# Optimization experiments

Hardware: AMD Instinct MI355X
Metric: run time of the kernel (lower is better)

The kernel has to match this reference:

```python
import jax, jax.numpy as jnp
import numpy as np

B, T, D = 8, 2048, 512


def setup_inputs() -> dict:
    key = jax.random.key(0)
    k1, _ = jax.random.split(key)
    h = jax.random.normal(k1, (B, T, D), dtype=jnp.float32)
    k = jnp.ones((), dtype=jnp.float32)  # scalar learned decay param, init='ones'
    return {"h": h, "k": k}


def reference(h, k):
    # h: [B, T, D], k: scalar
    Tn = h.shape[1]
    h_cum = jnp.cumsum(h, axis=1)                                   # [B,T,D]
    h_prev = jnp.pad(h[:, :-1, :], ((0, 0), (1, 0), (0, 0)))        # shift right by 1
    delta = h_cum - h_prev
    delta_mag = jnp.linalg.norm(delta, axis=-1)                      # [B,T]
    t = jnp.arange(Tn)[:, None]
    j = jnp.arange(Tn)[None, :]
    dist = jnp.abs(t - j).astype(jnp.float32)
    decay = jnp.exp(-jax.nn.softplus(k) * dist) * (j <= t)           # [T,T] causal decay
    # importance_{b,i,j} = delta_mag_{b,i} * decay_{i,j}; factor delta_mag out of einsum
    context = jnp.einsum('ij,bjd->bid', decay, h)                    # [B,T,D]
    return jnp.abs(delta_mag[..., None] * context)
```

## Files before the change

### kernel.cpp

```cpp
#include <hip/hip_runtime.h>
#include <math.h>

#define BB 8
#define TT 2048
#define DD 512
#define LL 16
#define CC (TT / LL)
#define D4 (DD / 4)

__device__ __forceinline__ float get_s(const float* kp) {
    float k = *kp;
    return (k > 20.0f) ? k : log1pf(expf(k));
}

__global__ __launch_bounds__(D4) void k1_chunk(
    const float* __restrict__ h, const float* __restrict__ kp,
    float* __restrict__ csum, float* __restrict__ cend)
{
    const int blk = blockIdx.x;
    const int b = blk / CC, c = blk % CC;
    const int tid = threadIdx.x;
    const float a = expf(-get_s(kp));

    const float4* hp = reinterpret_cast<const float4*>(h)
                     + (size_t)(b * TT + c * LL) * D4 + tid;

    float4 x[LL];
    #pragma unroll
    for (int i = 0; i < LL; i++) x[i] = hp[(size_t)i * D4];

    float sx = 0.f, sy = 0.f, sz = 0.f, sw = 0.f;
    float ex = 0.f, ey = 0.f, ez = 0.f, ew = 0.f;
    #pragma unroll
    for (int i = 0; i < LL; i++) {
        sx += x[i].x; sy += x[i].y; sz += x[i].z; sw += x[i].w;
        ex = fmaf(a, ex, x[i].x);
        ey = fmaf(a, ey, x[i].y);
        ez = fmaf(a, ez, x[i].z);
        ew = fmaf(a, ew, x[i].w);
    }
    const size_t w = (size_t)(b * CC + c) * D4 + tid;
    reinterpret_cast<float4*>(csum)[w] = make_float4(sx, sy, sz, sw);
    reinterpret_cast<float4*>(cend)[w] = make_float4(ex, ey, ez, ew);
}

__global__ __launch_bounds__(64) void k2_scan(
    const float* __restrict__ csum, const float* __restrict__ cend,
    const float* __restrict__ kp,
    float* __restrict__ coff, float* __restrict__ ccar)
{
    const int g = blockIdx.x * 64 + threadIdx.x;
    const int b = g >> 9;
    const int d = g & (DD - 1);
    const float s  = get_s(kp);
    const float aL = expf(-s * (float)LL);

    const size_t base = (size_t)b * CC * DD + d;
    float co = 0.f, cc = 0.f;
    #pragma unroll 8
    for (int c = 0; c < CC; c++) {
        const size_t idx = base + (size_t)c * DD;
        float sv = csum[idx];
        float ev = cend[idx];
        coff[idx] = co;
        ccar[idx] = cc;
        co += sv;
        cc = fmaf(aL, cc, ev);
    }
}

__global__ __launch_bounds__(D4) void k3_out(
    const float* __restrict__ h, const float* __restrict__ kp,
    const float* __restrict__ coff, const float* __restrict__ ccar,
    float* __restrict__ out)
{
    const int blk = blockIdx.x;
    const int b = blk / CC, c = blk % CC;
    const int tid = threadIdx.x;
    const int wave = tid >> 6, lane = tid & 63;
    const float a = expf(-get_s(kp));

    const int t0 = c * LL;
    const float4* hp = reinterpret_cast<const float4*>(h)
                     + (size_t)(b * TT + t0) * D4 + tid;

    float4 x[LL];
    #pragma unroll
    for (int i = 0; i < LL; i++) x[i] = hp[(size_t)i * D4];

    const size_t ci = (size_t)(b * CC + c) * D4 + tid;
    float4 co = reinterpret_cast<const float4*>(coff)[ci];
    float4 cc = reinterpret_cast<const float4*>(ccar)[ci];

    float px = 0.f, py = 0.f, pz = 0.f, pw = 0.f;
    if (t0 > 0) {
        float4 pv = hp[-(size_t)D4];
        px = pv.x; py = pv.y; pz = pv.z; pw = pv.w;
    }

    __shared__ float m2s[2][LL];
    __shared__ float mags[LL];

    float cox = co.x, coy = co.y, coz = co.z, cow = co.w;
    #pragma unroll
    for (int i = 0; i < LL; i++) {
        cox += x[i].x; coy += x[i].y; coz += x[i].z; cow += x[i].w;
        float dx = cox - px, dy = coy - py, dz = coz - pz, dw = cow - pw;
        float r = dx * dx + dy * dy + dz * dz + dw * dw;
        px = x[i].x; py = x[i].y; pz = x[i].z; pw = x[i].w;
        #pragma unroll
        for (int m = 32; m > 0; m >>= 1) r += __shfl_xor(r, m, 64);
        if (lane == 0) m2s[wave][i] = r;
    }
    __syncthreads();
    if (tid < LL) mags[tid] = sqrtf(m2s[0][tid] + m2s[1][tid]);
    __syncthreads();

    float4* op = reinterpret_cast<float4*>(out)
               + (size_t)(b * TT + t0) * D4 + tid;
    float ccx = cc.x, ccy = cc.y, ccz = cc.z, ccw = cc.w;
    #pragma unroll
    for (int i = 0; i < LL; i++) {
        ccx = fmaf(a, ccx, x[i].x);
        ccy = fmaf(a, ccy, x[i].y);
        ccz = fmaf(a, ccz, x[i].z);
        ccw = fmaf(a, ccw, x[i].w);
        float m = mags[i];
        op[(size_t)i * D4] = make_float4(fabsf(m * ccx), fabsf(m * ccy),
                                         fabsf(m * ccz), fabsf(m * ccw));
    }
}

extern "C" void kernel_launch(void* const* d_in, const int* in_sizes, int n_in,
                              void* d_out, int out_size, void* d_ws, size_t ws_size,
                              hipStream_t stream) {
    const float* h  = (const float*)d_in[0];
    const float* kp = (const float*)d_in[1];
    float* out = (float*)d_out;

    const size_t NS = (size_t)BB * CC * DD;
    float* csum = (float*)d_ws;
    float* cend = csum + NS;
    float* coff = cend + NS;
    float* ccar = coff + NS;

    k1_chunk<<<dim3(BB * CC), dim3(D4), 0, stream>>>(h, kp, csum, cend);
    k2_scan <<<dim3(BB * DD / 64), dim3(64), 0, stream>>>(csum, cend, kp, coff, ccar);
    k3_out  <<<dim3(BB * CC), dim3(D4), 0, stream>>>(h, kp, coff, ccar, out);
}
```

Baseline: 106.2 us.

## Fuse chunk, scan and output kernels into single-pass decoupled look-back scan

Replaces the three-kernel chunk/scan/output pipeline with one kernel where each chunk block publishes its local aggregate, looks back over predecessor chunks via flags to build its inclusive prefix (both plain sum and decayed carry), then computes outputs. This removes the second read of h, the serial per-column scan kernel, and extra launches. It adds inter-block spin-waiting that relies on forward-progress of earlier blocks and a memset of the flag array each call.

```diff
diff --git a/kernel.cpp b/kernel.cpp
--- a/kernel.cpp
+++ b/kernel.cpp
@@ -13,17 +13,30 @@
     return (k > 20.0f) ? k : log1pf(expf(k));
 }
 
-__global__ __launch_bounds__(D4) void k1_chunk(
+__global__ __launch_bounds__(D4) void k_fused(
     const float* __restrict__ h, const float* __restrict__ kp,
-    float* __restrict__ csum, float* __restrict__ cend)
+    float* __restrict__ csum, float* __restrict__ cend,
+    float* __restrict__ psum, float* __restrict__ pend,
+    int*   __restrict__ flags,
+    float* __restrict__ out)
 {
     const int blk = blockIdx.x;
     const int b = blk / CC, c = blk % CC;
     const int tid = threadIdx.x;
-    const float a = expf(-get_s(kp));
+    const int wave = tid >> 6, lane = tid & 63;
+    const float s  = get_s(kp);
+    const float a  = expf(-s);
+    const float aL = expf(-s * (float)LL);
 
+    const int t0 = c * LL;
     const float4* hp = reinterpret_cast<const float4*>(h)
-                     + (size_t)(b * TT + c * LL) * D4 + tid;
+                     + (size_t)(b * TT + t0) * D4 + tid;
+
+    float px = 0.f, py = 0.f, pz = 0.f, pw = 0.f;
+    if (t0 > 0) {
+        float4 pv = hp[-(size_t)D4];
+        px = pv.x; py = pv.y; pz = pv.z; pw = pv.w;
+    }
 
     float4 x[LL];
     #pragma unroll
@@ -39,69 +52,67 @@
         ez = fmaf(a, ez, x[i].z);
         ew = fmaf(a, ew, x[i].w);
     }
-    const size_t w = (size_t)(b * CC + c) * D4 + tid;
-    reinterpret_cast<float4*>(csum)[w] = make_float4(sx, sy, sz, sw);
-    reinterpret_cast<float4*>(cend)[w] = make_float4(ex, ey, ez, ew);
-}
 
-__global__ __launch_bounds__(64) void k2_scan(
-    const float* __restrict__ csum, const float* __restrict__ cend,
-    const float* __restrict__ kp,
-    float* __restrict__ coff, float* __restrict__ ccar)
-{
-    const int g = blockIdx.x * 64 + threadIdx.x;
-    const int b = g >> 9;
-    const int d = g & (DD - 1);
-    const float s  = get_s(kp);
-    const float aL = expf(-s * (float)LL);
+    const size_t ci = (size_t)blk * D4 + tid;
 
-    const size_t base = (size_t)b * CC * DD + d;
-    float co = 0.f, cc = 0.f;
-    #pragma unroll 8
-    for (int c = 0; c < CC; c++) {
-        const size_t idx = base + (size_t)c * DD;
-        float sv = csum[idx];
-        float ev = cend[idx];
-        coff[idx] = co;
-        ccar[idx] = cc;
-        co += sv;
-        cc = fmaf(aL, cc, ev);
+    if (c > 0) {
+        reinterpret_cast<float4*>(csum)[ci] = make_float4(sx, sy, sz, sw);
+        reinterpret_cast<float4*>(cend)[ci] = make_float4(ex, ey, ez, ew);
+        __syncthreads();
+        if (tid == 0)
+            __hip_atomic_store(flags + blk, 1, __ATOMIC_RELEASE,
+                               __HIP_MEMORY_SCOPE_AGENT);
     }
-}
 
-__global__ __launch_bounds__(D4) void k3_out(
-    const float* __restrict__ h, const float* __restrict__ kp,
-    const float* __restrict__ coff, const float* __restrict__ ccar,
-    float* __restrict__ out)
-{
-    const int blk = blockIdx.x;
-    const int b = blk / CC, c = blk % CC;
-    const int tid = threadIdx.x;
-    const int wave = tid >> 6, lane = tid & 63;
-    const float a = expf(-get_s(kp));
+    float cox = 0.f, coy = 0.f, coz = 0.f, cow = 0.f;
+    float ccx = 0.f, ccy = 0.f, ccz = 0.f, ccw = 0.f;
+    if (c > 0) {
+        float w = 1.f;
+        for (int cp = c - 1; cp >= 0; --cp) {
+            const int fidx = b * CC + cp;
+            int f = __hip_atomic_load(flags + fidx, __ATOMIC_ACQUIRE,
+                                      __HIP_MEMORY_SCOPE_AGENT);
+            while (f == 0) {
+                __builtin_amdgcn_s_sleep(1);
+                f = __hip_atomic_load(flags + fidx, __ATOMIC_ACQUIRE,
+                                      __HIP_MEMORY_SCOPE_AGENT);
+            }
+            const size_t pi = (size_t)fidx * D4 + tid;
+            if (f == 2) {
+                float4 pv = reinterpret_cast<const float4*>(psum)[pi];
+                float4 yv = reinterpret_cast<const float4*>(pend)[pi];
+                cox += pv.x; coy += pv.y; coz += pv.z; cow += pv.w;
+                ccx = fmaf(w, yv.x, ccx);
+                ccy = fmaf(w, yv.y, ccy);
+                ccz = fmaf(w, yv.z, ccz);
+                ccw = fmaf(w, yv.w, ccw);
+                break;
+            } else {
+                float4 sv = reinterpret_cast<const float4*>(csum)[pi];
+                float4 ev = reinterpret_cast<const float4*>(cend)[pi];
+                cox += sv.x; coy += sv.y; coz += sv.z; cow += sv.w;
+                ccx = fmaf(w, ev.x, ccx);
+                ccy = fmaf(w, ev.y, ccy);
+                ccz = fmaf(w, ev.z, ccz);
+                ccw = fmaf(w, ev.w, ccw);
+                w *= aL;
+            }
+        }
+    }
 
-    const int t0 = c * LL;
-    const float4* hp = reinterpret_cast<const float4*>(h)
-                     + (size_t)(b * TT + t0) * D4 + tid;
-
-    float4 x[LL];
-    #pragma unroll
-    for (int i = 0; i < LL; i++) x[i] = hp[(size_t)i * D4];
-
-    const size_t ci = (size_t)(b * CC + c) * D4 + tid;
-    float4 co = reinterpret_cast<const float4*>(coff)[ci];
-    float4 cc = reinterpret_cast<const float4*>(ccar)[ci];
-
-    float px = 0.f, py = 0.f, pz = 0.f, pw = 0.f;
-    if (t0 > 0) {
-        float4 pv = hp[-(size_t)D4];
-        px = pv.x; py = pv.y; pz = pv.z; pw = pv.w;
-    }
+    reinterpret_cast<float4*>(psum)[ci] =
+        make_float4(cox + sx, coy + sy, coz + sz, cow + sw);
+    reinterpret_cast<float4*>(pend)[ci] =
+        make_float4(fmaf(aL, ccx, ex), fmaf(aL, ccy, ey),
+                    fmaf(aL, ccz, ez), fmaf(aL, ccw, ew));
+    __syncthreads();
+    if (tid == 0)
+        __hip_atomic_store(flags + blk, 2, __ATOMIC_RELEASE,
+                           __HIP_MEMORY_SCOPE_AGENT);
 
     __shared__ float m2s[2][LL];
     __shared__ float mags[LL];
 
-    float cox = co.x, coy = co.y, coz = co.z, cow = co.w;
     #pragma unroll
     for (int i = 0; i < LL; i++) {
         cox += x[i].x; coy += x[i].y; coz += x[i].z; cow += x[i].w;
@@ -118,7 +129,6 @@
 
     float4* op = reinterpret_cast<float4*>(out)
                + (size_t)(b * TT + t0) * D4 + tid;
-    float ccx = cc.x, ccy = cc.y, ccz = cc.z, ccw = cc.w;
     #pragma unroll
     for (int i = 0; i < LL; i++) {
         ccx = fmaf(a, ccx, x[i].x);
@@ -141,10 +151,11 @@
     const size_t NS = (size_t)BB * CC * DD;
     float* csum = (float*)d_ws;
     float* cend = csum + NS;
-    float* coff = cend + NS;
-    float* ccar = coff + NS;
+    float* psum = cend + NS;
+    float* pend = psum + NS;
+    int*   flags = (int*)(pend + NS);
 
-    k1_chunk<<<dim3(BB * CC), dim3(D4), 0, stream>>>(h, kp, csum, cend);
-    k2_scan <<<dim3(BB * DD / 64), dim3(64), 0, stream>>>(csum, cend, kp, coff, ccar);
-    k3_out  <<<dim3(BB * CC), dim3(D4), 0, stream>>>(h, kp, coff, ccar, out);
+    hipMemsetAsync(flags, 0, (size_t)BB * CC * sizeof(int), stream);
+    k_fused<<<dim3(BB * CC), dim3(D4), 0, stream>>>(
+        h, kp, csum, cend, psum, pend, flags, out);
 }
```

Result: slower. 351.6 us (+231.0%).

## Halve chunk length, scan chunk prefixes in place, batch wave reductions

Applied to the files above, without the earlier changes.

Shrinks the chunk length from 16 to 8 so the chunk and output kernels launch twice as many smaller blocks with lower register use. The middle scan now overwrites its input buffers in place and uses 128-thread blocks with deeper unrolling. The output kernel batches all per-timestep wave shuffles and removes one block barrier. In exchange the serial scan has twice as many steps over fewer blocks, and workspace traffic grows.

```diff
diff --git a/kernel.cpp b/kernel.cpp
--- a/kernel.cpp
+++ b/kernel.cpp
@@ -4,9 +4,10 @@
 #define BB 8
 #define TT 2048
 #define DD 512
-#define LL 16
+#define LL 8
 #define CC (TT / LL)
 #define D4 (DD / 4)
+#define NBLK (BB * CC)
 
 __device__ __forceinline__ float get_s(const float* kp) {
     float k = *kp;
@@ -39,17 +40,16 @@
         ez = fmaf(a, ez, x[i].z);
         ew = fmaf(a, ew, x[i].w);
     }
-    const size_t w = (size_t)(b * CC + c) * D4 + tid;
+    const size_t w = (size_t)blk * D4 + tid;
     reinterpret_cast<float4*>(csum)[w] = make_float4(sx, sy, sz, sw);
     reinterpret_cast<float4*>(cend)[w] = make_float4(ex, ey, ez, ew);
 }
 
-__global__ __launch_bounds__(64) void k2_scan(
-    const float* __restrict__ csum, const float* __restrict__ cend,
-    const float* __restrict__ kp,
-    float* __restrict__ coff, float* __restrict__ ccar)
+__global__ __launch_bounds__(128) void k2_scan(
+    float* __restrict__ csum, float* __restrict__ cend,
+    const float* __restrict__ kp)
 {
-    const int g = blockIdx.x * 64 + threadIdx.x;
+    const int g = blockIdx.x * 128 + threadIdx.x;
     const int b = g >> 9;
     const int d = g & (DD - 1);
     const float s  = get_s(kp);
@@ -57,13 +57,13 @@
 
     const size_t base = (size_t)b * CC * DD + d;
     float co = 0.f, cc = 0.f;
-    #pragma unroll 8
+    #pragma unroll 16
     for (int c = 0; c < CC; c++) {
         const size_t idx = base + (size_t)c * DD;
         float sv = csum[idx];
         float ev = cend[idx];
-        coff[idx] = co;
-        ccar[idx] = cc;
+        csum[idx] = co;
+        cend[idx] = cc;
         co += sv;
         cc = fmaf(aL, cc, ev);
     }
@@ -84,13 +84,9 @@
     const float4* hp = reinterpret_cast<const float4*>(h)
                      + (size_t)(b * TT + t0) * D4 + tid;
 
-    float4 x[LL];
-    #pragma unroll
-    for (int i = 0; i < LL; i++) x[i] = hp[(size_t)i * D4];
-
-    const size_t ci = (size_t)(b * CC + c) * D4 + tid;
-    float4 co = reinterpret_cast<const float4*>(coff)[ci];
-    float4 cc = reinterpret_cast<const float4*>(ccar)[ci];
+    const size_t ci = (size_t)blk * D4 + tid;
+    float4 co4 = reinterpret_cast<const float4*>(coff)[ci];
+    float4 cc4 = reinterpret_cast<const float4*>(ccar)[ci];
 
     float px = 0.f, py = 0.f, pz = 0.f, pw = 0.f;
     if (t0 > 0) {
@@ -98,34 +94,47 @@
         px = pv.x; py = pv.y; pz = pv.z; pw = pv.w;
     }
 
-    __shared__ float m2s[2][LL];
-    __shared__ float mags[LL];
+    float4 x[LL];
+    #pragma unroll
+    for (int i = 0; i < LL; i++) x[i] = hp[(size_t)i * D4];
 
-    float cox = co.x, coy = co.y, coz = co.z, cow = co.w;
+    float r[LL];
+    float cox = co4.x, coy = co4.y, coz = co4.z, cow = co4.w;
     #pragma unroll
     for (int i = 0; i < LL; i++) {
         cox += x[i].x; coy += x[i].y; coz += x[i].z; cow += x[i].w;
         float dx = cox - px, dy = coy - py, dz = coz - pz, dw = cow - pw;
-        float r = dx * dx + dy * dy + dz * dz + dw * dw;
+        r[i] = dx * dx + dy * dy + dz * dz + dw * dw;
         px = x[i].x; py = x[i].y; pz = x[i].z; pw = x[i].w;
+    }
+
+    #pragma unroll
+    for (int m = 1; m < 64; m <<= 1) {
         #pragma unroll
-        for (int m = 32; m > 0; m >>= 1) r += __shfl_xor(r, m, 64);
-        if (lane == 0) m2s[wave][i] = r;
+        for (int i = 0; i < LL; i++) r[i] += __shfl_xor(r[i], m, 64);
+    }
+
+    __shared__ float part[2][LL];
+    if (lane == 0) {
+        #pragma unroll
+        for (int i = 0; i < LL; i++) part[wave][i] = r[i];
     }
     __syncthreads();
-    if (tid < LL) mags[tid] = sqrtf(m2s[0][tid] + m2s[1][tid]);
-    __syncthreads();
+
+    float mag[LL];
+    #pragma unroll
+    for (int i = 0; i < LL; i++) mag[i] = sqrtf(part[0][i] + part[1][i]);
 
     float4* op = reinterpret_cast<float4*>(out)
                + (size_t)(b * TT + t0) * D4 + tid;
-    float ccx = cc.x, ccy = cc.y, ccz = cc.z, ccw = cc.w;
+    float ccx = cc4.x, ccy = cc4.y, ccz = cc4.z, ccw = cc4.w;
     #pragma unroll
     for (int i = 0; i < LL; i++) {
         ccx = fmaf(a, ccx, x[i].x);
         ccy = fmaf(a, ccy, x[i].y);
         ccz = fmaf(a, ccz, x[i].z);
         ccw = fmaf(a, ccw, x[i].w);
-        float m = mags[i];
+        float m = mag[i];
         op[(size_t)i * D4] = make_float4(fabsf(m * ccx), fabsf(m * ccy),
                                          fabsf(m * ccz), fabsf(m * ccw));
     }
@@ -141,10 +150,8 @@
     const size_t NS = (size_t)BB * CC * DD;
     float* csum = (float*)d_ws;
     float* cend = csum + NS;
-    float* coff = cend + NS;
-    float* ccar = coff + NS;
 
-    k1_chunk<<<dim3(BB * CC), dim3(D4), 0, stream>>>(h, kp, csum, cend);
-    k2_scan <<<dim3(BB * DD / 64), dim3(64), 0, stream>>>(csum, cend, kp, coff, ccar);
-    k3_out  <<<dim3(BB * CC), dim3(D4), 0, stream>>>(h, kp, coff, ccar, out);
+    k1_chunk<<<dim3(NBLK), dim3(D4), 0, stream>>>(h, kp, csum, cend);
+    k2_scan <<<dim3(BB * DD / 128), dim3(128), 0, stream>>>(csum, cend, kp);
+    k3_out  <<<dim3(NBLK), dim3(D4), 0, stream>>>(h, kp, csum, cend, out);
 }
```

After: 110.1 us. 3.7% more time.
